# Kernel tuning notes

Measured on AMD Instinct MI355X. Metric: run time of the kernel, lower is better.

## Reference

```python
import jax, jax.numpy as jnp
import numpy as np
from jax import lax

S = 2048      # seq_len
E = 512       # loc_emb_size
H = 512       # hidden_size
V = 50000     # loc_size
WIN = 11      # window: j in [i-10, i]
LAMBDA_T = 0.1
LAMBDA_S = 50.0
DAY = 86400.0


def setup_inputs() -> dict:
    key = jax.random.key(0)
    ks = jax.random.split(key, 10)
    loc = jax.random.randint(ks[0], (S, 1), 0, V)
    # monotonically increasing timestamps spanning ~1 week
    tim = jnp.sort(jax.random.uniform(ks[1], (S,), dtype=jnp.float32) * (7.0 * DAY))
    coord = jax.random.uniform(ks[2], (S, 2), dtype=jnp.float32)
    emb = jax.random.normal(ks[3], (V, E), dtype=jnp.float32) * 0.02
    s_e = 1.0 / np.sqrt(E)
    s_h = 1.0 / np.sqrt(H)
    W_ih = jax.random.normal(ks[4], (3 * H, E), dtype=jnp.float32) * s_e
    W_hh = jax.random.normal(ks[5], (3 * H, H), dtype=jnp.float32) * s_h
    b_ih = jnp.zeros((3 * H,), dtype=jnp.float32)
    b_hh = jnp.zeros((3 * H,), dtype=jnp.float32)
    fc_w = jax.random.normal(ks[6], (V, H), dtype=jnp.float32) * s_h
    fc_b = jnp.zeros((V,), dtype=jnp.float32)
    return {"loc": loc, "tim": tim, "coord": coord, "emb": emb,
            "W_ih": W_ih, "W_hh": W_hh, "b_ih": b_ih, "b_hh": b_hh,
            "fc_w": fc_w, "fc_b": fc_b}


def _gru(x, W_ih, W_hh, b_ih, b_hh):
    # x: [S, E] -> out: [S, H]; PyTorch GRU equations (batch=1, 1 layer)
    xg = x @ W_ih.T + b_ih  # [S, 3H] precomputed input gates
    h0 = jnp.zeros((H,), dtype=x.dtype)

    def step(h, xg_t):
        hg = h @ W_hh.T + b_hh
        xr, xz, xn = jnp.split(xg_t, 3)
        hr, hz, hn = jnp.split(hg, 3)
        r = jax.nn.sigmoid(xr + hr)
        z = jax.nn.sigmoid(xz + hz)
        n = jnp.tanh(xn + r * hn)
        h_new = (1.0 - z) * n + z * h
        return h_new, h_new

    _, out = lax.scan(step, h0, xg)
    return out


def _flashback_core(out, tim, coord):
    # windowed spatiotemporal-decay weighted aggregation, fully vectorized
    i = jnp.arange(S)
    d = jnp.arange(WIN)                      # offsets 0..10
    j = i[:, None] - d[None, :]
    valid = j >= 0
    jc = jnp.maximum(j, 0)
    dt = tim[:, None] - tim[jc]
    diff = coord[:, None, :] - coord[jc]
    sq = jnp.sum(diff * diff, axis=-1)
    ds = jnp.sqrt(jnp.where(sq > 0, sq, 1.0)) * (sq > 0)  # safe norm (grad 0 at 0)
    f_t = (jnp.cos(dt * (2.0 * np.pi / DAY)) + 1.0) * 0.5 * jnp.exp(-(dt / DAY) * LAMBDA_T)
    f_s = jnp.exp(-ds * LAMBDA_S)
    w = jnp.where(valid, f_t * f_s + 1e-10, 0.0)
    out_w = jnp.einsum('sw,swh->sh', w, out[jc]) / jnp.sum(w, axis=1, keepdims=True)
    return out_w


def reference(loc, tim, coord, emb, W_ih, W_hh, b_ih, b_hh, fc_w, fc_b):
    x = emb[loc[:, 0]]                       # [S, E] (dropout is identity in eval)
    out = _gru(x, W_ih, W_hh, b_ih, b_hh)    # [S, H]
    out_w = _flashback_core(out, tim, coord) # [S, H]
    h = jax.nn.selu(out_w)
    y = h @ fc_w.T + fc_b                    # [S, V]
    return jax.nn.log_softmax(y, axis=-1)
```

## Files before the change

### kernel.cpp

```cpp
#include <hip/hip_runtime.h>
#include <math.h>

#define S_DIM 2048
#define H_DIM 512
#define V_DIM 50000
#define K_DIM 512
#define WINN 11
#define GRU_G 32

typedef __attribute__((ext_vector_type(4))) float f32x4;
typedef __attribute__((ext_vector_type(8))) __bf16 bf16x8;
typedef __attribute__((ext_vector_type(4))) unsigned int u32x4;

__device__ __forceinline__ unsigned int f2bf(float f) {
  union { float f; unsigned int u; } v; v.f = f;
  return (v.u + 0x7fffu + ((v.u >> 16) & 1u)) >> 16;
}
__device__ __forceinline__ unsigned int pack2(float a, float b) {
  return f2bf(a) | (f2bf(b) << 16);
}
__device__ __forceinline__ unsigned long long ld_pair(const unsigned long long* p) {
  return __hip_atomic_load(p, __ATOMIC_RELAXED, __HIP_MEMORY_SCOPE_AGENT);
}

__global__ void k_zero(int* p, int n) {
  int i = blockIdx.x * 256 + threadIdx.x;
  if (i < n) p[i] = 0;
}

__global__ void k_swizzle(const float* __restrict__ src, unsigned short* __restrict__ dst,
                          int rows_valid, int nchunks) {
  int c = blockIdx.x * 256 + threadIdx.x;
  if (c >= nchunks) return;
  int vt  = c >> 13;
  int m   = (c >> 6) & 127;
  int ktq = c & 63;
  int v = vt * 128 + m;
  f32x4 a = {0, 0, 0, 0}, b = {0, 0, 0, 0};
  if (v < rows_valid) {
    const float* s = src + (size_t)v * K_DIM + ktq * 8;
    a = *(const f32x4*)s;
    b = *(const f32x4*)(s + 4);
  }
  u32x4 pk;
  pk.x = pack2(a.x, a.y); pk.y = pack2(a.z, a.w);
  pk.z = pack2(b.x, b.y); pk.w = pack2(b.z, b.w);
  int kt = ktq >> 2, q = ktq & 3;
  int cd = vt * 8192 + kt * 512 + q * 128 + m;
  *(u32x4*)(dst + (size_t)cd * 8) = pk;
}

__global__ void k_gather(const float* __restrict__ emb, const int* __restrict__ loc,
                         unsigned short* __restrict__ dst) {
  int c = blockIdx.x * 256 + threadIdx.x;
  int st  = c >> 13;
  int m   = (c >> 6) & 127;
  int ktq = c & 63;
  int s = st * 128 + m;
  int l = loc[s];
  const float* sp = emb + (size_t)l * K_DIM + ktq * 8;
  f32x4 a = *(const f32x4*)sp;
  f32x4 b = *(const f32x4*)(sp + 4);
  u32x4 pk;
  pk.x = pack2(a.x, a.y); pk.y = pack2(a.z, a.w);
  pk.z = pack2(b.x, b.y); pk.w = pack2(b.z, b.w);
  int kt = ktq >> 2, q = ktq & 3;
  int cd = st * 8192 + kt * 512 + q * 128 + m;
  *(u32x4*)(dst + (size_t)cd * 8) = pk;
}

__global__ __launch_bounds__(256) void k_gemm(const unsigned short* __restrict__ A,
                                              const unsigned short* __restrict__ B,
                                              const float* __restrict__ bias,
                                              float* __restrict__ C, int ldc, int nvalid,
                                              float* lse_acc) {
  __shared__ __align__(16) unsigned short Als[4096];
  __shared__ __align__(16) unsigned short Bls[4096];
  int t = threadIdx.x;
  int ntile = blockIdx.x, mtile = blockIdx.y;
  const unsigned short* Ab = A + (size_t)mtile * 65536;
  const unsigned short* Bb = B + (size_t)ntile * 65536;
  int wid = t >> 6, lane = t & 63;
  int qm = wid >> 1, qn = wid & 1;
  int l15 = lane & 15, q4 = lane >> 4;
  f32x4 acc[4][4];
#pragma unroll
  for (int i = 0; i < 4; i++)
#pragma unroll
    for (int j = 0; j < 4; j++) acc[i][j] = (f32x4){0, 0, 0, 0};

  for (int kt = 0; kt < 16; ++kt) {
    __syncthreads();
    ((u32x4*)Als)[t]       = ((const u32x4*)(Ab + kt * 4096))[t];
    ((u32x4*)Als)[t + 256] = ((const u32x4*)(Ab + kt * 4096))[t + 256];
    ((u32x4*)Bls)[t]       = ((const u32x4*)(Bb + kt * 4096))[t];
    ((u32x4*)Bls)[t + 256] = ((const u32x4*)(Bb + kt * 4096))[t + 256];
    __syncthreads();
    bf16x8 af[4], bfr[4];
#pragma unroll
    for (int i = 0; i < 4; i++)
      af[i] = *(const bf16x8*)(&Als[(q4 * 128 + qm * 64 + i * 16 + l15) * 8]);
#pragma unroll
    for (int j = 0; j < 4; j++)
      bfr[j] = *(const bf16x8*)(&Bls[(q4 * 128 + qn * 64 + j * 16 + l15) * 8]);
#pragma unroll
    for (int i = 0; i < 4; i++)
#pragma unroll
      for (int j = 0; j < 4; j++)
        acc[i][j] = __builtin_amdgcn_mfma_f32_16x16x32_bf16(af[i], bfr[j], acc[i][j], 0, 0, 0);
  }

  int m0 = mtile * 128 + qm * 64;
  int n0 = ntile * 128 + qn * 64;
  float bv[4];
#pragma unroll
  for (int j = 0; j < 4; j++) {
    int n = n0 + j * 16 + l15;
    bv[j] = (n < nvalid) ? bias[n] : 0.f;
  }
#pragma unroll
  for (int i = 0; i < 4; i++) {
#pragma unroll
    for (int e = 0; e < 4; e++) {
      int r = m0 + i * 16 + q4 * 4 + e;
      float rs = 0.f;
#pragma unroll
      for (int j = 0; j < 4; j++) {
        int n = n0 + j * 16 + l15;
        if (n < nvalid) {
          float y = acc[i][j][e] + bv[j];
          C[(size_t)r * ldc + n] = y;
          rs += expf(y);
        }
      }
      if (lse_acc) {
        rs += __shfl_xor(rs, 1, 64);
        rs += __shfl_xor(rs, 2, 64);
        rs += __shfl_xor(rs, 4, 64);
        rs += __shfl_xor(rs, 8, 64);
        if (l15 == 0) atomicAdd(&lse_acc[r], rs);
      }
    }
  }
}

__global__ __launch_bounds__(256, 1) void k_gru(const float* __restrict__ W_hh,
                                                const float* __restrict__ b_hh,
                                                const float* __restrict__ xg,
                                                unsigned long long* h_pairs,
                                                float* __restrict__ out_gru) {
  __shared__ __align__(16) float h_lds[2][512];
  __shared__ float hg_l[48];
  int wg = blockIdx.x;
  int t = threadIdx.x;
  int wv = t >> 6;
  int lane = t & 63;
  int cg = lane >> 4;
  int kq = lane & 15;
  bool act = (wv < 3);
  f32x4 wr[4][8];
  float bhh[4];
  if (act) {
#pragma unroll
    for (int c = 0; c < 4; c++) {
      int grow = wv * 512 + wg * 16 + cg * 4 + c;
      const float* wsrc = W_hh + (size_t)grow * K_DIM + kq * 32;
#pragma unroll
      for (int v = 0; v < 8; v++) wr[c][v] = *(const f32x4*)(wsrc + v * 4);
      bhh[c] = b_hh[grow];
    }
  }
  int col = wg * 16 + t;
  float ho = 0.f;
  int j0 = t >> 2;
  int wp0 = ((j0 ^ ((j0 >> 3) & 7)) << 2) | (t & 3);
  int j1 = (t + 256) >> 2;
  int wp1 = ((j1 ^ ((j1 >> 3) & 7)) << 2) | (t & 3);

  for (int s = 0; s < S_DIM; ++s) {
    float xr = 0.f, xz = 0.f, xn = 0.f;
    if (t < 16) {
      const float* xrow = xg + (size_t)s * 1536;
      xr = xrow[col]; xz = xrow[512 + col]; xn = xrow[1024 + col];
    }

    unsigned long long* p0 = h_pairs + (size_t)(s & 1) * 512 + t;
    unsigned long long* p1 = p0 + 256;
    unsigned long long u0 = ld_pair(p0), u1 = ld_pair(p1);
    while ((unsigned)(u0 >> 32) != (unsigned)s) u0 = ld_pair(p0);
    while ((unsigned)(u1 >> 32) != (unsigned)s) u1 = ld_pair(p1);
    union { unsigned u; float f; } c0, c1;
    c0.u = (unsigned)u0; c1.u = (unsigned)u1;
    float* hb = h_lds[s & 1];
    hb[wp0] = c0.f;
    hb[wp1] = c1.f;
    __syncthreads();

    float pr[4] = {0.f, 0.f, 0.f, 0.f};
    if (act) {
      const f32x4* h4 = (const f32x4*)hb;
#pragma unroll
      for (int v = 0; v < 8; v++) {
        f32x4 hv = h4[(kq * 8 + v) ^ (kq & 7)];
#pragma unroll
        for (int c = 0; c < 4; c++) {
          pr[c] += wr[c][v].x * hv.x + wr[c][v].y * hv.y +
                   wr[c][v].z * hv.z + wr[c][v].w * hv.w;
        }
      }
    }
#pragma unroll
    for (int c = 0; c < 4; c++) {
      pr[c] += __shfl_xor(pr[c], 1, 64);
      pr[c] += __shfl_xor(pr[c], 2, 64);
      pr[c] += __shfl_xor(pr[c], 4, 64);
      pr[c] += __shfl_xor(pr[c], 8, 64);
    }
    if (act && kq == 0) {
#pragma unroll
      for (int c = 0; c < 4; c++) hg_l[wv * 16 + cg * 4 + c] = pr[c] + bhh[c];
    }
    __syncthreads();

    if (t < 16) {
      float hr = hg_l[t], hz = hg_l[16 + t], hn = hg_l[32 + t];
      float rg = 1.f / (1.f + __expf(-(xr + hr)));
      float zg = 1.f / (1.f + __expf(-(xz + hz)));
      float e2 = __expf(2.f * (xn + rg * hn));
      float nn = 1.f - 2.f / (e2 + 1.f);
      float hnew = (1.f - zg) * nn + zg * ho;
      union { float f; unsigned u; } pv; pv.f = hnew;
      unsigned long long up = ((unsigned long long)(unsigned)(s + 1) << 32) |
                              (unsigned long long)pv.u;
      __hip_atomic_store(h_pairs + (size_t)((s + 1) & 1) * 512 + col, up,
                         __ATOMIC_RELAXED, __HIP_MEMORY_SCOPE_AGENT);
      out_gru[(size_t)s * H_DIM + col] = hnew;
      ho = hnew;
    }
  }
}

__global__ __launch_bounds__(256) void k_flash(const float* __restrict__ out_gru,
                                               const float* __restrict__ tim,
                                               const float* __restrict__ coord,
                                               unsigned short* __restrict__ hs_sw) {
  __shared__ float hsl[512];
  int s = blockIdx.x;
  int t = threadIdx.x;
  float w[WINN];
  float ts = tim[s];
  float cx = coord[s * 2], cy = coord[s * 2 + 1];
  float wsum = 0.f;
#pragma unroll
  for (int d = 0; d < WINN; ++d) {
    int j = s - d;
    float wd = 0.f;
    if (j >= 0) {
      float dt = ts - tim[j];
      float dx = cx - coord[j * 2], dy = cy - coord[j * 2 + 1];
      float sq = dx * dx + dy * dy;
      float ds = sq > 0.f ? sqrtf(sq) : 0.f;
      float ft = (cosf(dt * 7.2722052166430395e-05f) + 1.f) * 0.5f *
                 expf(dt * -1.1574074074074074e-06f);
      float fs = expf(-50.f * ds);
      wd = ft * fs + 1e-10f;
    }
    w[d] = wd;
    wsum += wd;
  }
  float inv = 1.f / wsum;
  for (int h = t; h < H_DIM; h += 256) {
    float a = 0.f;
#pragma unroll
    for (int d = 0; d < WINN; ++d) {
      int j = s - d;
      if (j >= 0) a += w[d] * out_gru[(size_t)j * H_DIM + h];
    }
    a *= inv;
    float o = a > 0.f ? 1.0507009873554805f * a
                      : 1.7580993408473766f * expm1f(a);
    hsl[h] = o;
  }
  __syncthreads();
  if (t < 64) {
    int kt = t >> 2, q = t & 3;
    const float* p = &hsl[t * 8];
    u32x4 pk;
    pk.x = pack2(p[0], p[1]); pk.y = pack2(p[2], p[3]);
    pk.z = pack2(p[4], p[5]); pk.w = pack2(p[6], p[7]);
    int st = s >> 7, m = s & 127;
    int cd = st * 8192 + kt * 512 + q * 128 + m;
    *(u32x4*)(hs_sw + (size_t)cd * 8) = pk;
  }
}

__global__ __launch_bounds__(256) void k_sub(float* __restrict__ Y,
                                             const float* __restrict__ lse) {
  int i = blockIdx.x * 256 + threadIdx.x;
  const int n4 = S_DIM * (V_DIM / 4);
  if (i >= n4) return;
  int row = (i * 4) / V_DIM;
  f32x4* Y4 = (f32x4*)Y;
  f32x4 v = Y4[i];
  float l = logf(lse[row]);
  v.x -= l; v.y -= l; v.z -= l; v.w -= l;
  Y4[i] = v;
}

extern "C" void kernel_launch(void* const* d_in, const int* in_sizes, int n_in,
                              void* d_out, int out_size, void* d_ws, size_t ws_size,
                              hipStream_t stream) {
  const int*   loc   = (const int*)d_in[0];
  const float* tim   = (const float*)d_in[1];
  const float* coord = (const float*)d_in[2];
  const float* emb   = (const float*)d_in[3];
  const float* W_ih  = (const float*)d_in[4];
  const float* W_hh  = (const float*)d_in[5];
  const float* b_ih  = (const float*)d_in[6];
  const float* b_hh  = (const float*)d_in[7];
  const float* fc_w  = (const float*)d_in[8];
  const float* fc_b  = (const float*)d_in[9];
  float* Y = (float*)d_out;

  char* w = (char*)d_ws;
  unsigned long long* h_pairs = (unsigned long long*)(w);
  float* lse     = (float*)(w + 8192);
  float* xg      = (float*)(w + 16384);
  float* out_gru = (float*)(w + 12599296);
  unsigned short* x_sw   = (unsigned short*)(w + 16793600);
  unsigned short* wih_sw = (unsigned short*)(w + 18890752);
  unsigned short* hs_sw  = (unsigned short*)(w + 20463616);
  unsigned short* fcw_sw = (unsigned short*)(w + 22560768);

  k_zero<<<16, 256, 0, stream>>>((int*)w, 4096);
  k_swizzle<<<12512, 256, 0, stream>>>(fc_w, fcw_sw, 50000, 391 * 8192);
  k_swizzle<<<384, 256, 0, stream>>>(W_ih, wih_sw, 1536, 12 * 8192);
  k_gather<<<512, 256, 0, stream>>>(emb, loc, x_sw);
  dim3 gx(12, 16);
  k_gemm<<<gx, 256, 0, stream>>>(x_sw, wih_sw, b_ih, xg, 1536, 1536, nullptr);
  k_gru<<<GRU_G, 256, 0, stream>>>(W_hh, b_hh, xg, h_pairs, out_gru);
  k_flash<<<2048, 256, 0, stream>>>(out_gru, tim, coord, hs_sw);
  dim3 gy(391, 16);
  k_gemm<<<gy, 256, 0, stream>>>(hs_sw, fcw_sw, fc_b, Y, 50000, 50000, lse);
  k_sub<<<100000, 256, 0, stream>>>(Y, lse);
}
```

Baseline: 4.899 ms.

## Restructure GRU step so each thread owns all three gates, removing second barrier

Each 16-lane group now computes all three gate dot products for one hidden column, so the gate nonlinearity runs in the lane that holds the shuffle-reduced sums. This drops the shared hg buffer and the second __syncthreads per timestep. The polling of the published hidden state now uses a single 16-byte uncached load covering two (value, step) pairs instead of two 8-byte atomic loads. The wider load relies on both pairs being observed together, and the inline asm with an embedded waitcnt limits how the compiler can schedule around it.

```diff
diff --git a/kernel.cpp b/kernel.cpp
--- a/kernel.cpp
+++ b/kernel.cpp
@@ -9,6 +9,7 @@
 #define GRU_G 32
 
 typedef __attribute__((ext_vector_type(4))) float f32x4;
+typedef __attribute__((ext_vector_type(2))) float f32x2;
 typedef __attribute__((ext_vector_type(8))) __bf16 bf16x8;
 typedef __attribute__((ext_vector_type(4))) unsigned int u32x4;
 
@@ -19,8 +20,11 @@
 __device__ __forceinline__ unsigned int pack2(float a, float b) {
   return f2bf(a) | (f2bf(b) << 16);
 }
-__device__ __forceinline__ unsigned long long ld_pair(const unsigned long long* p) {
-  return __hip_atomic_load(p, __ATOMIC_RELAXED, __HIP_MEMORY_SCOPE_AGENT);
+__device__ __forceinline__ u32x4 ld_quad(const unsigned long long* p) {
+  u32x4 r;
+  asm volatile("global_load_dwordx4 %0, %1, off sc0 sc1\n\ts_waitcnt vmcnt(0)"
+               : "=v"(r) : "v"(p) : "memory");
+  return r;
 }
 
 __global__ void k_zero(int* p, int n) {
@@ -150,87 +154,67 @@
                                                 unsigned long long* h_pairs,
                                                 float* __restrict__ out_gru) {
   __shared__ __align__(16) float h_lds[2][512];
-  __shared__ float hg_l[48];
   int wg = blockIdx.x;
   int t = threadIdx.x;
-  int wv = t >> 6;
-  int lane = t & 63;
-  int cg = lane >> 4;
-  int kq = lane & 15;
-  bool act = (wv < 3);
-  f32x4 wr[4][8];
-  float bhh[4];
-  if (act) {
-#pragma unroll
-    for (int c = 0; c < 4; c++) {
-      int grow = wv * 512 + wg * 16 + cg * 4 + c;
-      const float* wsrc = W_hh + (size_t)grow * K_DIM + kq * 32;
-#pragma unroll
-      for (int v = 0; v < 8; v++) wr[c][v] = *(const f32x4*)(wsrc + v * 4);
-      bhh[c] = b_hh[grow];
-    }
-  }
-  int col = wg * 16 + t;
+  int cg = t >> 4;
+  int kq = t & 15;
+  int col = wg * 16 + cg;
+  bool pub = (kq == 0);
+  f32x4 wr[3][8];
+  float bh0, bh1, bh2;
+#pragma unroll
+  for (int gate = 0; gate < 3; gate++) {
+    int grow = gate * 512 + col;
+    const float* wsrc = W_hh + (size_t)grow * K_DIM + kq * 32;
+#pragma unroll
+    for (int v = 0; v < 8; v++) wr[gate][v] = *(const f32x4*)(wsrc + v * 4);
+  }
+  bh0 = b_hh[col]; bh1 = b_hh[512 + col]; bh2 = b_hh[1024 + col];
   float ho = 0.f;
-  int j0 = t >> 2;
-  int wp0 = ((j0 ^ ((j0 >> 3) & 7)) << 2) | (t & 3);
-  int j1 = (t + 256) >> 2;
-  int wp1 = ((j1 ^ ((j1 >> 3) & 7)) << 2) | (t & 3);
+  int j = t >> 1;
+  int pj = j ^ ((j >> 3) & 7);
+  int stoff = pj * 4 + (t & 1) * 2;
 
   for (int s = 0; s < S_DIM; ++s) {
+    unsigned su = (unsigned)s;
     float xr = 0.f, xz = 0.f, xn = 0.f;
-    if (t < 16) {
+    if (pub) {
       const float* xrow = xg + (size_t)s * 1536;
       xr = xrow[col]; xz = xrow[512 + col]; xn = xrow[1024 + col];
     }
 
-    unsigned long long* p0 = h_pairs + (size_t)(s & 1) * 512 + t;
-    unsigned long long* p1 = p0 + 256;
-    unsigned long long u0 = ld_pair(p0), u1 = ld_pair(p1);
-    while ((unsigned)(u0 >> 32) != (unsigned)s) u0 = ld_pair(p0);
-    while ((unsigned)(u1 >> 32) != (unsigned)s) u1 = ld_pair(p1);
-    union { unsigned u; float f; } c0, c1;
-    c0.u = (unsigned)u0; c1.u = (unsigned)u1;
+    const unsigned long long* p = h_pairs + (size_t)(s & 1) * 512 + t * 2;
+    u32x4 q = ld_quad(p);
+    while (q.y != su || q.w != su) q = ld_quad(p);
+    union { unsigned u; float f; } a0, a1;
+    a0.u = q.x; a1.u = q.z;
     float* hb = h_lds[s & 1];
-    hb[wp0] = c0.f;
-    hb[wp1] = c1.f;
+    *(f32x2*)(&hb[stoff]) = (f32x2){a0.f, a1.f};
     __syncthreads();
 
-    float pr[4] = {0.f, 0.f, 0.f, 0.f};
-    if (act) {
-      const f32x4* h4 = (const f32x4*)hb;
-#pragma unroll
-      for (int v = 0; v < 8; v++) {
-        f32x4 hv = h4[(kq * 8 + v) ^ (kq & 7)];
-#pragma unroll
-        for (int c = 0; c < 4; c++) {
-          pr[c] += wr[c][v].x * hv.x + wr[c][v].y * hv.y +
-                   wr[c][v].z * hv.z + wr[c][v].w * hv.w;
-        }
-      }
-    }
-#pragma unroll
-    for (int c = 0; c < 4; c++) {
-      pr[c] += __shfl_xor(pr[c], 1, 64);
-      pr[c] += __shfl_xor(pr[c], 2, 64);
-      pr[c] += __shfl_xor(pr[c], 4, 64);
-      pr[c] += __shfl_xor(pr[c], 8, 64);
-    }
-    if (act && kq == 0) {
-#pragma unroll
-      for (int c = 0; c < 4; c++) hg_l[wv * 16 + cg * 4 + c] = pr[c] + bhh[c];
-    }
-    __syncthreads();
-
-    if (t < 16) {
-      float hr = hg_l[t], hz = hg_l[16 + t], hn = hg_l[32 + t];
+    float p0 = 0.f, p1 = 0.f, p2 = 0.f;
+    const f32x4* h4 = (const f32x4*)hb;
+#pragma unroll
+    for (int v = 0; v < 8; v++) {
+      f32x4 hv = h4[(kq * 8 + v) ^ (kq & 7)];
+      p0 += wr[0][v].x * hv.x + wr[0][v].y * hv.y + wr[0][v].z * hv.z + wr[0][v].w * hv.w;
+      p1 += wr[1][v].x * hv.x + wr[1][v].y * hv.y + wr[1][v].z * hv.z + wr[1][v].w * hv.w;
+      p2 += wr[2][v].x * hv.x + wr[2][v].y * hv.y + wr[2][v].z * hv.z + wr[2][v].w * hv.w;
+    }
+    p0 += __shfl_xor(p0, 1, 64); p1 += __shfl_xor(p1, 1, 64); p2 += __shfl_xor(p2, 1, 64);
+    p0 += __shfl_xor(p0, 2, 64); p1 += __shfl_xor(p1, 2, 64); p2 += __shfl_xor(p2, 2, 64);
+    p0 += __shfl_xor(p0, 4, 64); p1 += __shfl_xor(p1, 4, 64); p2 += __shfl_xor(p2, 4, 64);
+    p0 += __shfl_xor(p0, 8, 64); p1 += __shfl_xor(p1, 8, 64); p2 += __shfl_xor(p2, 8, 64);
+
+    if (pub) {
+      float hr = p0 + bh0, hz = p1 + bh1, hn = p2 + bh2;
       float rg = 1.f / (1.f + __expf(-(xr + hr)));
       float zg = 1.f / (1.f + __expf(-(xz + hz)));
       float e2 = __expf(2.f * (xn + rg * hn));
       float nn = 1.f - 2.f / (e2 + 1.f);
       float hnew = (1.f - zg) * nn + zg * ho;
       union { float f; unsigned u; } pv; pv.f = hnew;
-      unsigned long long up = ((unsigned long long)(unsigned)(s + 1) << 32) |
+      unsigned long long up = ((unsigned long long)(su + 1) << 32) |
                               (unsigned long long)pv.u;
       __hip_atomic_store(h_pairs + (size_t)((s + 1) & 1) * 512 + col, up,
                          __ATOMIC_RELAXED, __HIP_MEMORY_SCOPE_AGENT);
```

Result: no change. 4.916 ms (+0.3%).
